# Optimization experiments

Hardware: AMD Instinct MI355X
Metric: run time of the kernel (lower is better)

The kernel has to match this reference:

```python
import jax, jax.numpy as jnp
import numpy as np

L, H, P = 16384, 1024, 512  # seq len, model width, state size (conj_sym: P = ssm_size//2)
DT_MIN, DT_MAX = 1e-3, 1e-1
STEP_RESCALE = 1.0


def setup_inputs() -> dict:
    key = jax.random.key(0)
    ks = jax.random.split(key, 7)
    input_sequence = jax.random.normal(ks[0], (L, H), dtype=jnp.float32)
    # Lambda: stable diagonal (Re < 0), like DPLR-HiPPO (Re = -0.5, spread imag parts)
    Lambda_re = -0.5 - jax.random.uniform(ks[1], (P,), dtype=jnp.float32)
    Lambda_im = 10.0 * jax.random.normal(ks[2], (P,), dtype=jnp.float32)
    # B (P,H,2) and C (H,P,2): real/imag stacked parameterization
    B = jax.random.normal(ks[3], (P, H, 2), dtype=jnp.float32) / np.float32(np.sqrt(H))
    C = jax.random.normal(ks[4], (H, P, 2), dtype=jnp.float32) / np.float32(np.sqrt(P))
    D = jax.random.normal(ks[5], (H,), dtype=jnp.float32)
    log_step = (jax.random.uniform(ks[6], (P, 1), dtype=jnp.float32)
                * (np.log(DT_MAX) - np.log(DT_MIN)) + np.log(DT_MIN)).astype(jnp.float32)
    return {"input_sequence": input_sequence, "Lambda_re": Lambda_re,
            "Lambda_im": Lambda_im, "B": B, "C": C, "D": D, "log_step": log_step}


def _binop(q_i, q_j):
    # diagonal linear recurrence composition; elementwise, so works on stacked arrays
    A_i, b_i = q_i
    A_j, b_j = q_j
    return (A_j * A_i, A_j * b_i + b_j)


def reference(input_sequence, Lambda_re, Lambda_im, B, C, D, log_step):
    Lambda = Lambda_re + 1j * Lambda_im                      # (P,) complex64
    B_tilde = B[..., 0] + 1j * B[..., 1]                     # (P,H)
    C_tilde = C[..., 0] + 1j * C[..., 1]                     # (H,P)
    Delta = STEP_RESCALE * jnp.exp(log_step[:, 0])           # (P,)
    # ZOH discretization
    Lambda_bar = jnp.exp(Lambda * Delta)                     # (P,)
    B_bar = ((Lambda_bar - 1.0) / Lambda)[:, None] * B_tilde # (P,H)
    # per-step scan elements
    Lambda_elements = jnp.broadcast_to(Lambda_bar, (input_sequence.shape[0], P))
    Bu_elements = jnp.einsum('lh,ph->lp', input_sequence, B_bar)  # (L,P) complex
    _, xs = jax.lax.associative_scan(_binop, (Lambda_elements, Bu_elements))
    # conj_sym readout: 2 * Re(C x)
    ys = 2.0 * jnp.einsum('lp,hp->lh', xs, C_tilde).real     # (L,H) float32
    return ys + input_sequence * D
```

## Files before the change

kernel.cpp:

```cpp
#include <hip/hip_runtime.h>
#include <math.h>

#define LL 16384
#define HH 1024
#define PP 512
#define NP2 1024
#define CHUNK 64
#define NCHUNK 256

#define BM2 256
#define BN2 256
#define SUBK 32
#define REG_U16 16384

typedef unsigned short u16;
typedef __attribute__((ext_vector_type(8))) short bf16x8;
typedef __attribute__((ext_vector_type(4))) float f32x4;

__device__ __forceinline__ u16 f2bf(float f) {
    unsigned u = __float_as_uint(f);
    unsigned r = 0x7fffu + ((u >> 16) & 1u);
    return (u16)((u + r) >> 16);
}
__device__ __forceinline__ float bf2f(u16 x) {
    return __uint_as_float(((unsigned)x) << 16);
}

__device__ __forceinline__ void gload_lds16(const void* g, void* l) {
    __builtin_amdgcn_global_load_lds(
        (const __attribute__((address_space(1))) unsigned int*)g,
        (__attribute__((address_space(3))) unsigned int*)l, 16, 0, 0);
}

#define SB0 __builtin_amdgcn_sched_barrier(0)

__global__ __launch_bounds__(256) void k_prep(
        const float* __restrict__ B, const float* __restrict__ C,
        const float* __restrict__ u, const float* __restrict__ lre,
        const float* __restrict__ lim, const float* __restrict__ logstep,
        u16* __restrict__ bb, u16* __restrict__ cp, u16* __restrict__ ub,
        float* __restrict__ lbre, float* __restrict__ lbim,
        float* __restrict__ ltre, float* __restrict__ ltim) {
    const int bx = blockIdx.x;
    if (bx < 2048) {
        int t = bx * 256 + threadIdx.x;
        int p = t >> 10, h = t & 1023;
        float2 b = ((const float2*)B)[t];
        float dt = expf(logstep[p]);
        float ar = lre[p], ai = lim[p];
        float e = expf(ar * dt);
        float s, c;
        sincosf(ai * dt, &s, &c);
        float nr = e * c - 1.0f, ni = e * s;
        float den = ar * ar + ai * ai;
        float gr = (nr * ar + ni * ai) / den;
        float gi = (ni * ar - nr * ai) / den;
        bb[(size_t)(2 * p) * HH + h]     = f2bf(gr * b.x - gi * b.y);
        bb[(size_t)(2 * p + 1) * HH + h] = f2bf(gr * b.y + gi * b.x);
    } else if (bx < 4096) {
        int t = (bx - 2048) * 256 + threadIdx.x;
        int h = t >> 9, p = t & 511;
        float2 c = ((const float2*)C)[t];
        cp[(size_t)h * NP2 + 2 * p]     = f2bf(c.x);
        cp[(size_t)h * NP2 + 2 * p + 1] = f2bf(-c.y);
    } else if (bx < 20480) {
        size_t i = ((size_t)(bx - 4096) * 256 + threadIdx.x) * 4;
        float4 v = *(const float4*)&u[i];
        unsigned lo = (unsigned)f2bf(v.x) | ((unsigned)f2bf(v.y) << 16);
        unsigned hi = (unsigned)f2bf(v.z) | ((unsigned)f2bf(v.w) << 16);
        *(uint2*)&ub[i] = make_uint2(lo, hi);
    } else {
        int p = (bx - 20480) * 256 + threadIdx.x;
        if (p < PP) {
            float dt = expf(logstep[p]);
            float ar = lre[p], ai = lim[p];
            float e = expf(ar * dt);
            float s, c;
            sincosf(ai * dt, &s, &c);
            float Lr = e * c, Li = e * s;
            lbre[p] = Lr; lbim[p] = Li;
            float tr = Lr, ti = Li;
            for (int i6 = 0; i6 < 6; i6++) {
                float rr = tr * tr - ti * ti;
                float mm = 2.0f * tr * ti;
                tr = rr; ti = mm;
            }
            ltre[p] = tr; ltim[p] = ti;
        }
    }
}

template<int FUSE>
__global__ __launch_bounds__(512, 2) void k_gemm2(
        const u16* __restrict__ A, const u16* __restrict__ Bt,
        void* __restrict__ outp, const int K,
        const u16* __restrict__ ubf, const float* __restrict__ Din,
        const float* __restrict__ lbre, const float* __restrict__ lbim,
        float* __restrict__ frO, float* __restrict__ fiO) {
    extern __shared__ u16 smem[];
    const int b = blockIdx.x;
    const int xcd = b & 7, sidx = b >> 3;
    const int m0 = (xcd * 8 + (sidx >> 2)) * BM2;
    const int n0 = (sidx & 3) * BN2;
    const int t = threadIdx.x;
    const int lane = t & 63, wid = t >> 6;
    const int wm = (wid >> 2) * 128, wn = (wid & 3) * 64;
    const int frow = lane & 15, quad = (lane >> 4) & 3;

    f32x4 acc[8][4];
    #pragma unroll
    for (int i = 0; i < 8; i++)
        #pragma unroll
        for (int j = 0; j < 4; j++) acc[i][j] = (f32x4){0.f, 0.f, 0.f, 0.f};

    const int sr = t >> 2, slot = t & 3;
    const int seg = slot ^ ((sr >> 1) & 3);
    const u16* gA = A + (size_t)(m0 + sr) * K + seg * 8;
    const u16* gB = Bt + (size_t)(n0 + sr) * K + seg * 8;
    const int ldst = sr * 32 + slot * 8;

    const int aoff = (wm + frow) * 32 + ((quad ^ ((frow >> 1) & 3)) * 8);
    const int boff = (wn + frow) * 32 + ((quad ^ ((frow >> 1) & 3)) * 8);

    const int NT = K / SUBK;

    {
        u16* d0 = smem + ldst;
        gload_lds16(gA,                     d0);
        gload_lds16(gA + (size_t)128 * K,   d0 + 4096);
        gload_lds16(gB,                     d0 + 8192);
        gload_lds16(gB + (size_t)128 * K,   d0 + 12288);
        u16* d1 = smem + REG_U16 + ldst;
        gload_lds16(gA + SUBK,                   d1);
        gload_lds16(gA + (size_t)128 * K + SUBK, d1 + 4096);
        gload_lds16(gB + SUBK,                   d1 + 8192);
        gload_lds16(gB + (size_t)128 * K + SUBK, d1 + 12288);
    }
    asm volatile("s_waitcnt vmcnt(4)" ::: "memory");
    SB0;
    __builtin_amdgcn_s_barrier();
    SB0;

    int rc = 0;
    int rs = 2;
    for (int s = 0; s < NT; ++s) {
        const u16* Ar = smem + rc * REG_U16;
        const u16* Br = Ar + 8192;
        const bool do_stage = (s + 2 < NT);
        const u16* gAs = gA + (size_t)(s + 2) * SUBK;
        const u16* gBs = gB + (size_t)(s + 2) * SUBK;
        u16* dS = smem + rs * REG_U16 + ldst;

        bf16x8 av0 = *(const bf16x8*)&Ar[aoff + 0 * 512];
        bf16x8 av1 = *(const bf16x8*)&Ar[aoff + 1 * 512];
        bf16x8 av2 = *(const bf16x8*)&Ar[aoff + 2 * 512];
        bf16x8 av3 = *(const bf16x8*)&Ar[aoff + 3 * 512];
        bf16x8 bv0 = *(const bf16x8*)&Br[boff + 0 * 512];
        bf16x8 bv1 = *(const bf16x8*)&Br[boff + 1 * 512];
        bf16x8 bv2 = *(const bf16x8*)&Br[boff + 2 * 512];
        bf16x8 bv3 = *(const bf16x8*)&Br[boff + 3 * 512];
        if (do_stage) {
            gload_lds16(gAs,                   dS);
            gload_lds16(gAs + (size_t)128 * K, dS + 4096);
        }
        SB0;
        __builtin_amdgcn_s_barrier();
        asm volatile("s_waitcnt lgkmcnt(0)" ::: "memory");
        SB0;
        __builtin_amdgcn_s_setprio(1);
        acc[0][0] = __builtin_amdgcn_mfma_f32_16x16x32_bf16(av0, bv0, acc[0][0], 0, 0, 0);
        acc[0][1] = __builtin_amdgcn_mfma_f32_16x16x32_bf16(av0, bv1, acc[0][1], 0, 0, 0);
        acc[0][2] = __builtin_amdgcn_mfma_f32_16x16x32_bf16(av0, bv2, acc[0][2], 0, 0, 0);
        acc[0][3] = __builtin_amdgcn_mfma_f32_16x16x32_bf16(av0, bv3, acc[0][3], 0, 0, 0);
        acc[1][0] = __builtin_amdgcn_mfma_f32_16x16x32_bf16(av1, bv0, acc[1][0], 0, 0, 0);
        acc[1][1] = __builtin_amdgcn_mfma_f32_16x16x32_bf16(av1, bv1, acc[1][1], 0, 0, 0);
        acc[1][2] = __builtin_amdgcn_mfma_f32_16x16x32_bf16(av1, bv2, acc[1][2], 0, 0, 0);
        acc[1][3] = __builtin_amdgcn_mfma_f32_16x16x32_bf16(av1, bv3, acc[1][3], 0, 0, 0);
        acc[2][0] = __builtin_amdgcn_mfma_f32_16x16x32_bf16(av2, bv0, acc[2][0], 0, 0, 0);
        acc[2][1] = __builtin_amdgcn_mfma_f32_16x16x32_bf16(av2, bv1, acc[2][1], 0, 0, 0);
        acc[2][2] = __builtin_amdgcn_mfma_f32_16x16x32_bf16(av2, bv2, acc[2][2], 0, 0, 0);
        acc[2][3] = __builtin_amdgcn_mfma_f32_16x16x32_bf16(av2, bv3, acc[2][3], 0, 0, 0);
        acc[3][0] = __builtin_amdgcn_mfma_f32_16x16x32_bf16(av3, bv0, acc[3][0], 0, 0, 0);
        acc[3][1] = __builtin_amdgcn_mfma_f32_16x16x32_bf16(av3, bv1, acc[3][1], 0, 0, 0);
        acc[3][2] = __builtin_amdgcn_mfma_f32_16x16x32_bf16(av3, bv2, acc[3][2], 0, 0, 0);
        acc[3][3] = __builtin_amdgcn_mfma_f32_16x16x32_bf16(av3, bv3, acc[3][3], 0, 0, 0);
        __builtin_amdgcn_s_setprio(0);
        SB0;
        __builtin_amdgcn_s_barrier();
        SB0;

        bf16x8 av4 = *(const bf16x8*)&Ar[aoff + 4 * 512];
        bf16x8 av5 = *(const bf16x8*)&Ar[aoff + 5 * 512];
        bf16x8 av6 = *(const bf16x8*)&Ar[aoff + 6 * 512];
        bf16x8 av7 = *(const bf16x8*)&Ar[aoff + 7 * 512];
        if (do_stage) {
            gload_lds16(gBs,                   dS + 8192);
            gload_lds16(gBs + (size_t)128 * K, dS + 12288);
        }
        SB0;
        __builtin_amdgcn_s_barrier();
        asm volatile("s_waitcnt lgkmcnt(0)" ::: "memory");
        SB0;
        __builtin_amdgcn_s_setprio(1);
        acc[4][0] = __builtin_amdgcn_mfma_f32_16x16x32_bf16(av4, bv0, acc[4][0], 0, 0, 0);
        acc[4][1] = __builtin_amdgcn_mfma_f32_16x16x32_bf16(av4, bv1, acc[4][1], 0, 0, 0);
        acc[4][2] = __builtin_amdgcn_mfma_f32_16x16x32_bf16(av4, bv2, acc[4][2], 0, 0, 0);
        acc[4][3] = __builtin_amdgcn_mfma_f32_16x16x32_bf16(av4, bv3, acc[4][3], 0, 0, 0);
        acc[5][0] = __builtin_amdgcn_mfma_f32_16x16x32_bf16(av5, bv0, acc[5][0], 0, 0, 0);
        acc[5][1] = __builtin_amdgcn_mfma_f32_16x16x32_bf16(av5, bv1, acc[5][1], 0, 0, 0);
        acc[5][2] = __builtin_amdgcn_mfma_f32_16x16x32_bf16(av5, bv2, acc[5][2], 0, 0, 0);
        acc[5][3] = __builtin_amdgcn_mfma_f32_16x16x32_bf16(av5, bv3, acc[5][3], 0, 0, 0);
        acc[6][0] = __builtin_amdgcn_mfma_f32_16x16x32_bf16(av6, bv0, acc[6][0], 0, 0, 0);
        acc[6][1] = __builtin_amdgcn_mfma_f32_16x16x32_bf16(av6, bv1, acc[6][1], 0, 0, 0);
        acc[6][2] = __builtin_amdgcn_mfma_f32_16x16x32_bf16(av6, bv2, acc[6][2], 0, 0, 0);
        acc[6][3] = __builtin_amdgcn_mfma_f32_16x16x32_bf16(av6, bv3, acc[6][3], 0, 0, 0);
        acc[7][0] = __builtin_amdgcn_mfma_f32_16x16x32_bf16(av7, bv0, acc[7][0], 0, 0, 0);
        acc[7][1] = __builtin_amdgcn_mfma_f32_16x16x32_bf16(av7, bv1, acc[7][1], 0, 0, 0);
        acc[7][2] = __builtin_amdgcn_mfma_f32_16x16x32_bf16(av7, bv2, acc[7][2], 0, 0, 0);
        acc[7][3] = __builtin_amdgcn_mfma_f32_16x16x32_bf16(av7, bv3, acc[7][3], 0, 0, 0);
        __builtin_amdgcn_s_setprio(0);
        if (s < NT - 2)       asm volatile("s_waitcnt vmcnt(4)" ::: "memory");
        else if (s == NT - 2) asm volatile("s_waitcnt vmcnt(0)" ::: "memory");
        SB0;
        __builtin_amdgcn_s_barrier();
        SB0;

        rc = (rc == 2) ? 0 : rc + 1;
        rs = (rs == 2) ? 0 : rs + 1;
    }

    if (FUSE) {
        float* Cout = (float*)outp;
        #pragma unroll
        for (int i = 0; i < 8; i++) {
            const int row = m0 + wm + i * 16 + quad * 4;
            #pragma unroll
            for (int j = 0; j < 4; j++) {
                const int col = n0 + wn + j * 16 + frow;
                const float dv = Din[col];
                f32x4 v = acc[i][j];
                #pragma unroll
                for (int r = 0; r < 4; r++) {
                    const size_t o = (size_t)(row + r) * 1024 + col;
                    Cout[o] = 2.0f * v[r] + bf2f(ubf[o]) * dv;
                }
            }
        }
    } else {
        u16* Cb = (u16*)outp;
        unsigned* sm32 = (unsigned*)smem;
        #pragma unroll
        for (int i = 0; i < 8; i++)
            #pragma unroll
            for (int j = 0; j < 4; j++) {
                f32x4 v = acc[i][j];
                #pragma unroll
                for (int r = 0; r < 4; r++)
                    smem[(wm + i * 16 + quad * 4 + r) * 256 + wn + j * 16 + frow]
                        = f2bf(v[r]);
            }
        __syncthreads();
        #pragma unroll
        for (int k = 0; k < 16; k++) {
            const int l = t + k * 512;
            const int row = l >> 5, c16 = (l & 31) * 8;
            *(uint4*)&Cb[(size_t)(m0 + row) * 1024 + n0 + c16] =
                ((const uint4*)smem)[l];
        }
        const int ch = t >> 7, q = t & 127;
        const int sp = (n0 >> 1) + q;
        const float sar = lbre[sp], sai = lbim[sp];
        float xr = 0.f, xi = 0.f;
        #pragma unroll 8
        for (int r = 0; r < 64; r++) {
            unsigned v = sm32[(ch * 64 + r) * 128 + q];
            float br = bf2f((u16)(v & 0xffff));
            float bi = bf2f((u16)(v >> 16));
            float nr = sar * xr - sai * xi + br;
            float ni = sar * xi + sai * xr + bi;
            xr = nr; xi = ni;
        }
        frO[((m0 >> 6) + ch) * PP + sp] = xr;
        fiO[((m0 >> 6) + ch) * PP + sp] = xi;
    }
}

__global__ __launch_bounds__(256) void k_scan2(
        const float* __restrict__ fr, const float* __restrict__ fi,
        const float* __restrict__ ltre, const float* __restrict__ ltim,
        float* __restrict__ cr, float* __restrict__ ci) {
    __shared__ float Ar[NCHUNK], Ai[NCHUNK], br[NCHUNK], bi[NCHUNK];
    const int p = blockIdx.x;
    const int c = threadIdx.x;
    const float lr = ltre[p], li = ltim[p];
    Ar[c] = lr; Ai[c] = li;
    br[c] = fr[c * PP + p];
    bi[c] = fi[c * PP + p];
    __syncthreads();
    #pragma unroll
    for (int d = 1; d < NCHUNK; d <<= 1) {
        float pAr = 0.f, pAi = 0.f, pbr = 0.f, pbi = 0.f;
        const bool has = (c >= d);
        if (has) { pAr = Ar[c-d]; pAi = Ai[c-d]; pbr = br[c-d]; pbi = bi[c-d]; }
        float cAr = Ar[c], cAi = Ai[c], cbr = br[c], cbi = bi[c];
        __syncthreads();
        if (has) {
            Ar[c] = cAr * pAr - cAi * pAi;
            Ai[c] = cAr * pAi + cAi * pAr;
            br[c] = cAr * pbr - cAi * pbi + cbr;
            bi[c] = cAr * pbi + cAi * pbr + cbi;
        }
        __syncthreads();
    }
    cr[c * PP + p] = (c == 0) ? 0.f : br[c-1];
    ci[c * PP + p] = (c == 0) ? 0.f : bi[c-1];
}

__global__ void k_scan3(unsigned* __restrict__ bu,
                        const float* __restrict__ lbre, const float* __restrict__ lbim,
                        const float* __restrict__ cr, const float* __restrict__ ci) {
    int p = blockIdx.x * 256 + threadIdx.x;
    int c = blockIdx.y;
    float ar = lbre[p], ai = lbim[p];
    float xr = cr[c * PP + p], xi = ci[c * PP + p];
    unsigned* b = bu + (size_t)c * CHUNK * PP + p;
    for (int j = 0; j < CHUNK; j += 4) {
        unsigned vv[4];
        vv[0] = b[0]; vv[1] = b[PP]; vv[2] = b[2 * PP]; vv[3] = b[3 * PP];
        unsigned w[4];
        #pragma unroll
        for (int q = 0; q < 4; q++) {
            float br = bf2f((u16)(vv[q] & 0xffff));
            float bi = bf2f((u16)(vv[q] >> 16));
            float nr = ar * xr - ai * xi + br;
            float ni = ar * xi + ai * xr + bi;
            xr = nr; xi = ni;
            w[q] = (unsigned)f2bf(xr) | ((unsigned)f2bf(xi) << 16);
        }
        b[0] = w[0]; b[PP] = w[1]; b[2 * PP] = w[2]; b[3 * PP] = w[3];
        b += 4 * PP;
    }
}

extern "C" void kernel_launch(void* const* d_in, const int* in_sizes, int n_in,
                              void* d_out, int out_size, void* d_ws, size_t ws_size,
                              hipStream_t stream) {
    const float* u       = (const float*)d_in[0];
    const float* lre     = (const float*)d_in[1];
    const float* lim     = (const float*)d_in[2];
    const float* B       = (const float*)d_in[3];
    const float* C       = (const float*)d_in[4];
    const float* D       = (const float*)d_in[5];
    const float* logstep = (const float*)d_in[6];
    float* out = (float*)d_out;

    float* w = (float*)d_ws;
    float* lbre = w + 1024;
    float* lbim = w + 1536;
    float* ltre = w + 2048;
    float* ltim = w + 2560;
    float* fr   = w + 4096;
    float* fi   = fr + NCHUNK * PP;
    float* cr   = fi + NCHUNK * PP;
    float* ci   = cr + NCHUNK * PP;
    u16*   bub  = (u16*)(w + (1 << 20));
    u16*   ub   = bub + (size_t)LL * NP2;
    u16*   bb   = ub + (size_t)LL * HH;
    u16*   cp   = bb + (size_t)NP2 * HH;

    static int attr_done = 0;
    if (!attr_done) {
        hipFuncSetAttribute(reinterpret_cast<const void*>(k_gemm2<0>),
                            hipFuncAttributeMaxDynamicSharedMemorySize, 131072);
        hipFuncSetAttribute(reinterpret_cast<const void*>(k_gemm2<1>),
                            hipFuncAttributeMaxDynamicSharedMemorySize, 131072);
        attr_done = 1;
    }

    k_prep<<<20482, 256, 0, stream>>>(B, C, u, lre, lim, logstep,
                                      bb, cp, ub, lbre, lbim, ltre, ltim);
    k_gemm2<0><<<(NP2 / BN2) * (LL / BM2), 512, 131072, stream>>>(
        ub, bb, bub, HH, nullptr, nullptr, lbre, lbim, fr, fi);
    k_scan2<<<PP, NCHUNK, 0, stream>>>(fr, fi, ltre, ltim, cr, ci);
    k_scan3<<<dim3(PP / 256, NCHUNK), 256, 0, stream>>>(
        (unsigned*)bub, lbre, lbim, cr, ci);
    k_gemm2<1><<<(HH / BN2) * (LL / BM2), 512, 131072, stream>>>(
        bub, cp, out, NP2, ub, D, nullptr, nullptr, nullptr, nullptr);
}
```

Baseline: 231.0 us.

## Fold chunk-carry scan into first GEMM via last-block atomic counter

Removes the separate k_scan2 launch. Each first-GEMM block now bumps an atomic counter after writing its chunk summaries, and the last block to finish runs a sequential 256-step carry scan over all 512 states. The change also uses nontemporal stores for the final output and unrolls the intra-chunk scan in k_scan3 to 8 steps. The gain is one fewer launch, paid for with a serial tail of 256 dependent steps on a single block and fence/atomic overhead in every block.

```diff
diff --git a/kernel.cpp b/kernel.cpp
--- a/kernel.cpp
+++ b/kernel.cpp
@@ -40,7 +40,8 @@
         const float* __restrict__ lim, const float* __restrict__ logstep,
         u16* __restrict__ bb, u16* __restrict__ cp, u16* __restrict__ ub,
         float* __restrict__ lbre, float* __restrict__ lbim,
-        float* __restrict__ ltre, float* __restrict__ ltim) {
+        float* __restrict__ ltre, float* __restrict__ ltim,
+        unsigned* __restrict__ cnt) {
     const int bx = blockIdx.x;
     if (bx < 2048) {
         int t = bx * 256 + threadIdx.x;
@@ -70,6 +71,7 @@
         unsigned hi = (unsigned)f2bf(v.z) | ((unsigned)f2bf(v.w) << 16);
         *(uint2*)&ub[i] = make_uint2(lo, hi);
     } else {
+        if (bx == 20480 && threadIdx.x == 0) *cnt = 0u;
         int p = (bx - 20480) * 256 + threadIdx.x;
         if (p < PP) {
             float dt = expf(logstep[p]);
@@ -96,7 +98,10 @@
         void* __restrict__ outp, const int K,
         const u16* __restrict__ ubf, const float* __restrict__ Din,
         const float* __restrict__ lbre, const float* __restrict__ lbim,
-        float* __restrict__ frO, float* __restrict__ fiO) {
+        float* __restrict__ frO, float* __restrict__ fiO,
+        const float* __restrict__ ltre, const float* __restrict__ ltim,
+        float* __restrict__ crO, float* __restrict__ ciO,
+        unsigned* __restrict__ cnt) {
     extern __shared__ u16 smem[];
     const int b = blockIdx.x;
     const int xcd = b & 7, sidx = b >> 3;
@@ -242,7 +247,8 @@
                 #pragma unroll
                 for (int r = 0; r < 4; r++) {
                     const size_t o = (size_t)(row + r) * 1024 + col;
-                    Cout[o] = 2.0f * v[r] + bf2f(ubf[o]) * dv;
+                    __builtin_nontemporal_store(
+                        2.0f * v[r] + bf2f(ubf[o]) * dv, &Cout[o]);
                 }
             }
         }
@@ -282,38 +288,38 @@
         }
         frO[((m0 >> 6) + ch) * PP + sp] = xr;
         fiO[((m0 >> 6) + ch) * PP + sp] = xi;
-    }
-}
-
-__global__ __launch_bounds__(256) void k_scan2(
-        const float* __restrict__ fr, const float* __restrict__ fi,
-        const float* __restrict__ ltre, const float* __restrict__ ltim,
-        float* __restrict__ cr, float* __restrict__ ci) {
-    __shared__ float Ar[NCHUNK], Ai[NCHUNK], br[NCHUNK], bi[NCHUNK];
-    const int p = blockIdx.x;
-    const int c = threadIdx.x;
-    const float lr = ltre[p], li = ltim[p];
-    Ar[c] = lr; Ai[c] = li;
-    br[c] = fr[c * PP + p];
-    bi[c] = fi[c * PP + p];
-    __syncthreads();
-    #pragma unroll
-    for (int d = 1; d < NCHUNK; d <<= 1) {
-        float pAr = 0.f, pAi = 0.f, pbr = 0.f, pbi = 0.f;
-        const bool has = (c >= d);
-        if (has) { pAr = Ar[c-d]; pAi = Ai[c-d]; pbr = br[c-d]; pbi = bi[c-d]; }
-        float cAr = Ar[c], cAi = Ai[c], cbr = br[c], cbi = bi[c];
+
+        __threadfence();
+        __shared__ unsigned is_last;
+        if (t == 0)
+            is_last = (atomicAdd(cnt, 1u) == gridDim.x - 1) ? 1u : 0u;
         __syncthreads();
-        if (has) {
-            Ar[c] = cAr * pAr - cAi * pAi;
-            Ai[c] = cAr * pAi + cAi * pAr;
-            br[c] = cAr * pbr - cAi * pbi + cbr;
-            bi[c] = cAr * pbi + cAi * pbr + cbi;
-        }
-        __syncthreads();
-    }
-    cr[c * PP + p] = (c == 0) ? 0.f : br[c-1];
-    ci[c * PP + p] = (c == 0) ? 0.f : bi[c-1];
+        if (is_last) {
+            __threadfence();
+            const int p = t;
+            const float lr = ltre[p], li = ltim[p];
+            float cxr = 0.f, cxi = 0.f;
+            for (int c = 0; c < NCHUNK; c += 4) {
+                float f0r = frO[(c + 0) * PP + p], f0i = fiO[(c + 0) * PP + p];
+                float f1r = frO[(c + 1) * PP + p], f1i = fiO[(c + 1) * PP + p];
+                float f2r = frO[(c + 2) * PP + p], f2i = fiO[(c + 2) * PP + p];
+                float f3r = frO[(c + 3) * PP + p], f3i = fiO[(c + 3) * PP + p];
+                float nr, ni;
+                crO[(c + 0) * PP + p] = cxr; ciO[(c + 0) * PP + p] = cxi;
+                nr = lr * cxr - li * cxi + f0r; ni = lr * cxi + li * cxr + f0i;
+                cxr = nr; cxi = ni;
+                crO[(c + 1) * PP + p] = cxr; ciO[(c + 1) * PP + p] = cxi;
+                nr = lr * cxr - li * cxi + f1r; ni = lr * cxi + li * cxr + f1i;
+                cxr = nr; cxi = ni;
+                crO[(c + 2) * PP + p] = cxr; ciO[(c + 2) * PP + p] = cxi;
+                nr = lr * cxr - li * cxi + f2r; ni = lr * cxi + li * cxr + f2i;
+                cxr = nr; cxi = ni;
+                crO[(c + 3) * PP + p] = cxr; ciO[(c + 3) * PP + p] = cxi;
+                nr = lr * cxr - li * cxi + f3r; ni = lr * cxi + li * cxr + f3i;
+                cxr = nr; cxi = ni;
+            }
+        }
+    }
 }
 
 __global__ void k_scan3(unsigned* __restrict__ bu,
@@ -324,12 +330,13 @@
     float ar = lbre[p], ai = lbim[p];
     float xr = cr[c * PP + p], xi = ci[c * PP + p];
     unsigned* b = bu + (size_t)c * CHUNK * PP + p;
-    for (int j = 0; j < CHUNK; j += 4) {
-        unsigned vv[4];
-        vv[0] = b[0]; vv[1] = b[PP]; vv[2] = b[2 * PP]; vv[3] = b[3 * PP];
-        unsigned w[4];
-        #pragma unroll
-        for (int q = 0; q < 4; q++) {
+    for (int j = 0; j < CHUNK; j += 8) {
+        unsigned vv[8];
+        #pragma unroll
+        for (int q = 0; q < 8; q++) vv[q] = b[q * PP];
+        unsigned w[8];
+        #pragma unroll
+        for (int q = 0; q < 8; q++) {
             float br = bf2f((u16)(vv[q] & 0xffff));
             float bi = bf2f((u16)(vv[q] >> 16));
             float nr = ar * xr - ai * xi + br;
@@ -337,8 +344,9 @@
             xr = nr; xi = ni;
             w[q] = (unsigned)f2bf(xr) | ((unsigned)f2bf(xi) << 16);
         }
-        b[0] = w[0]; b[PP] = w[1]; b[2 * PP] = w[2]; b[3 * PP] = w[3];
-        b += 4 * PP;
+        #pragma unroll
+        for (int q = 0; q < 8; q++) b[q * PP] = w[q];
+        b += 8 * PP;
     }
 }
 
@@ -359,6 +367,7 @@
     float* lbim = w + 1536;
     float* ltre = w + 2048;
     float* ltim = w + 2560;
+    unsigned* cnt = (unsigned*)(w + 3072);
     float* fr   = w + 4096;
     float* fi   = fr + NCHUNK * PP;
     float* cr   = fi + NCHUNK * PP;
@@ -378,12 +387,13 @@
     }
 
     k_prep<<<20482, 256, 0, stream>>>(B, C, u, lre, lim, logstep,
-                                      bb, cp, ub, lbre, lbim, ltre, ltim);
+                                      bb, cp, ub, lbre, lbim, ltre, ltim, cnt);
     k_gemm2<0><<<(NP2 / BN2) * (LL / BM2), 512, 131072, stream>>>(
-        ub, bb, bub, HH, nullptr, nullptr, lbre, lbim, fr, fi);
-    k_scan2<<<PP, NCHUNK, 0, stream>>>(fr, fi, ltre, ltim, cr, ci);
+        ub, bb, bub, HH, nullptr, nullptr, lbre, lbim, fr, fi,
+        ltre, ltim, cr, ci, cnt);
     k_scan3<<<dim3(PP / 256, NCHUNK), 256, 0, stream>>>(
         (unsigned*)bub, lbre, lbim, cr, ci);
     k_gemm2<1><<<(HH / BN2) * (LL / BM2), 512, 131072, stream>>>(
-        bub, cp, out, NP2, ub, D, nullptr, nullptr, nullptr, nullptr);
-}
+        bub, cp, out, NP2, ub, D, nullptr, nullptr, nullptr, nullptr,
+        nullptr, nullptr, nullptr, nullptr, nullptr);
+}
```

After: 351.8 us. 1.52x slower.
